# Optimization experiments

Measured on AMD Instinct MI355X. Metric: run time of the kernel, lower is better.

Reference implementation:

```python
import jax, jax.numpy as jnp
import numpy as np

B, S, H, N = 2, 2048, 1024, 16
D = H // N


def setup_inputs() -> dict:
    key = jax.random.key(0)
    k1, k2, k3 = jax.random.split(key, 3)
    # Xavier-uniform-ish init for projection weights
    lim_in = (6.0 / (H + 3 * H)) ** 0.5
    lim_out = (6.0 / (H + H)) ** 0.5
    return {
        "hidden_states": jax.random.normal(k1, (B, S, H), dtype=jnp.float32),
        "w_in": jax.random.uniform(k2, (3 * H, H), minval=-lim_in, maxval=lim_in, dtype=jnp.float32),
        "b_in": jnp.zeros((3 * H,), dtype=jnp.float32),
        "w_out": jax.random.uniform(k3, (H, H), minval=-lim_out, maxval=lim_out, dtype=jnp.float32),
        "b_out": jnp.zeros((H,), dtype=jnp.float32),
    }


def reference(hidden_states, w_in, b_in, w_out, b_out):
    b, s, h = hidden_states.shape
    qkv = hidden_states @ w_in.T + b_in  # [B,S,3H]
    q, k, v = jnp.split(qkv, 3, axis=-1)
    # [B,S,H] -> [B,N,S,D]
    def to_heads(x):
        return x.reshape(b, s, N, D).transpose(0, 2, 1, 3)
    q, k, v = to_heads(q), to_heads(k), to_heads(v)
    scale = D ** -0.5
    scores = jnp.einsum("bnqd,bnkd->bnqk", q, k) * scale  # [B,N,S,S]
    causal = jnp.triu(jnp.ones((s, s), dtype=bool), k=1)
    scores = jnp.where(causal, -jnp.inf, scores)
    attn = jax.nn.softmax(scores, axis=-1)
    out = jnp.einsum("bnqk,bnkd->bnqd", attn, v)  # [B,N,S,D]
    out = out.transpose(0, 2, 1, 3).reshape(b, s, h)
    return out @ w_out.T + b_out
```

## Files before the change

### kernel.cpp

```cpp
#include <hip/hip_runtime.h>
#include <hip/hip_bf16.h>

#define BB 2
#define SS 2048
#define HH 1024
#define NH 16
#define DD 64
#define H3 3072
#define MM (BB*SS)

typedef unsigned short u16;
typedef unsigned int u32;
typedef __attribute__((ext_vector_type(8))) short bf16x8;
typedef __attribute__((ext_vector_type(4))) float f32x4;
typedef __attribute__((ext_vector_type(16))) float f32x16;

__device__ __forceinline__ u16 f2bf(float f) {
    union { float f; u32 u; } v; v.f = f;
    u32 u = v.u;
    u += 0x7fffu + ((u >> 16) & 1u);
    return (u16)(u >> 16);
}
__device__ __forceinline__ float bf2f(u16 h) {
    union { u32 u; float f; } v; v.u = ((u32)h) << 16;
    return v.f;
}
__device__ __forceinline__ u32 pack2bf(float a, float b) {
    __hip_bfloat162 h = __float22bfloat162_rn(float2{a, b});
    u32 u; __builtin_memcpy(&u, &h, 4);
    return u;
}
__device__ __forceinline__ void gl_lds16(const void* g, void* l) {
    __builtin_amdgcn_global_load_lds(
        (const __attribute__((address_space(1))) u32*)g,
        (__attribute__((address_space(3))) u32*)l, 16, 0, 0);
}

__global__ void cvt3bf(const float4* __restrict__ s0, uint2* __restrict__ d0, int n0,
                       const float4* __restrict__ s1, uint2* __restrict__ d1, int n1,
                       const float4* __restrict__ s2, uint2* __restrict__ d2, int n2) {
    int i = blockIdx.x * blockDim.x + threadIdx.x;
    const int tot = n0 + n1 + n2;
    for (; i < tot; i += gridDim.x * blockDim.x) {
        const float4* s; uint2* d; int j;
        if (i < n0)            { s = s0; d = d0; j = i; }
        else if (i < n0 + n1)  { s = s1; d = d1; j = i - n0; }
        else                   { s = s2; d = d2; j = i - n0 - n1; }
        float4 v = s[j];
        uint2 o; o.x = pack2bf(v.x, v.y); o.y = pack2bf(v.z, v.w);
        d[j] = o;
    }
}

template<int BN, int MODE>
__global__ __launch_bounds__(256, 2)
void gemm_k2(const u16* __restrict__ A, const u16* __restrict__ Bbf,
             const u16* __restrict__ biasbf, void* __restrict__ Cptr,
             u16* __restrict__ Qo, u16* __restrict__ Ko, u16* __restrict__ Vto,
             int M, int Nn, int K)
{
    constexpr int NFR = BN / 32;
    __shared__ __align__(16) u16 Alds[128 * 32];
    __shared__ __align__(16) u16 Blds[BN * 32];
    const int tid = threadIdx.x;
    const int w = tid >> 6, lane = tid & 63, quad = lane >> 4, l16 = lane & 15;
    const int m0 = blockIdx.x * 128, n0 = blockIdx.y * BN;
    const int wm = w >> 1, wn = w & 1;
    const int rA4 = lane >> 2, c8b = (lane & 3) * 8;

    f32x4 acc[4][NFR] = {};

    for (int k0 = 0; k0 < K; k0 += 32) {
        __syncthreads();
#pragma unroll
        for (int q = 0; q < 2; ++q) {
            int row0 = w * 32 + q * 16;
            gl_lds16(&A[(size_t)(m0 + row0 + rA4) * K + k0 + c8b], &Alds[row0 * 32]);
        }
#pragma unroll
        for (int q = 0; q < BN / 64; ++q) {
            int row0 = w * (BN / 4) + q * 16;
            gl_lds16(&Bbf[(size_t)(n0 + row0 + rA4) * K + k0 + c8b], &Blds[row0 * 32]);
        }
        __syncthreads();

        bf16x8 af[4], bfr[NFR];
#pragma unroll
        for (int mi = 0; mi < 4; ++mi)
            af[mi] = *(const bf16x8*)&Alds[(wm * 64 + mi * 16 + l16) * 32 + quad * 8];
#pragma unroll
        for (int ni = 0; ni < NFR; ++ni)
            bfr[ni] = *(const bf16x8*)&Blds[(wn * (BN / 2) + ni * 16 + l16) * 32 + quad * 8];
#pragma unroll
        for (int mi = 0; mi < 4; ++mi)
#pragma unroll
            for (int ni = 0; ni < NFR; ++ni)
                acc[mi][ni] = __builtin_amdgcn_mfma_f32_16x16x32_bf16(
                    af[mi], bfr[ni], acc[mi][ni], 0, 0, 0);
    }

#pragma unroll
    for (int mi = 0; mi < 4; ++mi) {
        int row_b = m0 + wm * 64 + mi * 16 + quad * 4;
#pragma unroll
        for (int ni = 0; ni < NFR; ++ni) {
            int col = n0 + wn * (BN / 2) + ni * 16 + l16;
            float bv = bf2f(biasbf[col]);
            if constexpr (MODE == 1) {
#pragma unroll
                for (int i = 0; i < 4; ++i)
                    ((float*)Cptr)[(size_t)(row_b + i) * Nn + col] = acc[mi][ni][i] + bv;
            } else {
                if (col < 1024) {
#pragma unroll
                    for (int i = 0; i < 4; ++i)
                        Qo[(size_t)(row_b + i) * 1024 + col] =
                            f2bf((acc[mi][ni][i] + bv) * 0.125f);
                } else if (col < 2048) {
#pragma unroll
                    for (int i = 0; i < 4; ++i)
                        Ko[(size_t)(row_b + i) * 1024 + (col - 1024)] =
                            f2bf(acc[mi][ni][i] + bv);
                } else {
                    int d = col - 2048, hh = d >> 6, dd = d & 63;
                    int b = row_b >> 11, s = row_b & 2047;
                    u16 t0 = f2bf(acc[mi][ni][0] + bv), t1 = f2bf(acc[mi][ni][1] + bv);
                    u16 t2 = f2bf(acc[mi][ni][2] + bv), t3 = f2bf(acc[mi][ni][3] + bv);
                    uint2 pk; pk.x = (u32)t0 | ((u32)t1 << 16);
                    pk.y = (u32)t2 | ((u32)t3 << 16);
                    *(uint2*)&Vto[((size_t)((b * 16 + hh) * 64 + dd)) * 2048 + s] = pk;
                }
            }
        }
    }
}

__global__ __launch_bounds__(256, 2)
void attn_v4(const u16* __restrict__ Q, const u16* __restrict__ Kb,
             const u16* __restrict__ Vt, u16* __restrict__ attn_out) {
    const int qt = 15 - blockIdx.x, h = blockIdx.y, b = blockIdx.z;
    const int tid = threadIdx.x;
    const int w = tid >> 6, lane = tid & 63;
    const int l32 = lane & 31, h5 = lane >> 5;
    __shared__ __align__(16) u16 Klds[2][64 * 72];
    __shared__ __align__(16) u16 Vlds[2][64 * 72];
    __shared__ __align__(16) u16 Pb[4][32 * 72];
    const int r0 = tid >> 3, cc8 = (tid & 7) * 8;

    const int q0 = qt * 128;
    const int qw = q0 + w * 32;
    const int T = 2 * (qt + 1);

    const u16* Qb = Q  + (size_t)(b * SS) * 1024 + h * 64;
    const u16* Kg = Kb + (size_t)(b * SS) * 1024 + h * 64;
    const u16* Vg = Vt + (size_t)((b * 16 + h) * 64) * 2048;

    bf16x8 qf[4];
#pragma unroll
    for (int kt = 0; kt < 4; ++kt)
        qf[kt] = *(const bf16x8*)&Qb[(size_t)(qw + l32) * 1024 + kt * 16 + h5 * 8];

    f32x16 oacc[2] = {};
    float lp[16];
#pragma unroll
    for (int j = 0; j < 16; ++j) lp[j] = 0.f;

    uint4 kr0 = *(const uint4*)&Kg[(size_t)r0 * 1024 + cc8];
    uint4 kr1 = *(const uint4*)&Kg[(size_t)(r0 + 32) * 1024 + cc8];
    uint4 vr0 = *(const uint4*)&Vg[(size_t)r0 * 2048 + cc8];
    uint4 vr1 = *(const uint4*)&Vg[(size_t)(r0 + 32) * 2048 + cc8];
    *(uint4*)&Klds[0][r0 * 72 + cc8]        = kr0;
    *(uint4*)&Klds[0][(r0 + 32) * 72 + cc8] = kr1;
    *(uint4*)&Vlds[0][r0 * 72 + cc8]        = vr0;
    *(uint4*)&Vlds[0][(r0 + 32) * 72 + cc8] = vr1;

    for (int t = 0; t < T; ++t) {
        const int cur = t & 1;
        const int kv0 = t * 64;
        __syncthreads();
        if (t + 1 < T) {
            const int nv = kv0 + 64;
            kr0 = *(const uint4*)&Kg[(size_t)(nv + r0) * 1024 + cc8];
            kr1 = *(const uint4*)&Kg[(size_t)(nv + r0 + 32) * 1024 + cc8];
            vr0 = *(const uint4*)&Vg[(size_t)r0 * 2048 + nv + cc8];
            vr1 = *(const uint4*)&Vg[(size_t)(r0 + 32) * 2048 + nv + cc8];
        }
        f32x16 sacc[2] = {};
#pragma unroll
        for (int nt = 0; nt < 2; ++nt)
#pragma unroll
            for (int kt = 0; kt < 4; ++kt) {
                bf16x8 kf = *(const bf16x8*)
                    &Klds[cur][(nt * 32 + l32) * 72 + kt * 16 + h5 * 8];
                sacc[nt] = __builtin_amdgcn_mfma_f32_32x32x16_bf16(
                    qf[kt], kf, sacc[nt], 0, 0, 0);
            }
#pragma unroll
        for (int nt = 0; nt < 2; ++nt) {
            int colg = kv0 + nt * 32 + l32;
#pragma unroll
            for (int j = 0; j < 16; ++j) {
                int rl = (j & 3) + 8 * (j >> 2) + 4 * h5;
                float p = (colg <= qw + rl) ? __expf(sacc[nt][j]) : 0.f;
                lp[j] += p;
                Pb[w][rl * 72 + nt * 32 + l32] = f2bf(p);
            }
        }
#pragma unroll
        for (int kt = 0; kt < 4; ++kt) {
            bf16x8 pa = *(const bf16x8*)&Pb[w][l32 * 72 + kt * 16 + h5 * 8];
#pragma unroll
            for (int nt = 0; nt < 2; ++nt) {
                bf16x8 vf = *(const bf16x8*)
                    &Vlds[cur][(nt * 32 + l32) * 72 + kt * 16 + h5 * 8];
                oacc[nt] = __builtin_amdgcn_mfma_f32_32x32x16_bf16(
                    pa, vf, oacc[nt], 0, 0, 0);
            }
        }
        if (t + 1 < T) {
            const int nxt = cur ^ 1;
            *(uint4*)&Klds[nxt][r0 * 72 + cc8]        = kr0;
            *(uint4*)&Klds[nxt][(r0 + 32) * 72 + cc8] = kr1;
            *(uint4*)&Vlds[nxt][r0 * 72 + cc8]        = vr0;
            *(uint4*)&Vlds[nxt][(r0 + 32) * 72 + cc8] = vr1;
        }
    }

#pragma unroll
    for (int j = 0; j < 16; ++j) {
#pragma unroll
        for (int s = 1; s < 32; s <<= 1)
            lp[j] += __shfl_xor(lp[j], s, 64);
        lp[j] = 1.0f / lp[j];
    }
    u16* ob = attn_out + (size_t)(b * SS + qw) * 1024 + h * 64;
#pragma unroll
    for (int nt = 0; nt < 2; ++nt)
#pragma unroll
        for (int j = 0; j < 16; ++j) {
            int rl = (j & 3) + 8 * (j >> 2) + 4 * h5;
            ob[(size_t)rl * 1024 + nt * 32 + l32] = f2bf(oacc[nt][j] * lp[j]);
        }
}

extern "C" void kernel_launch(void* const* d_in, const int* in_sizes, int n_in,
                              void* d_out, int out_size, void* d_ws, size_t ws_size,
                              hipStream_t stream) {
    const float* hidden = (const float*)d_in[0];
    const float* w_in   = (const float*)d_in[1];
    const float* b_in   = (const float*)d_in[2];
    const float* w_out  = (const float*)d_in[3];
    const float* b_out  = (const float*)d_in[4];
    float* out = (float*)d_out;

    char* ws = (char*)d_ws;
    u16* hid_bf  = (u16*)d_out;
    u16* wi_bf   = (u16*)ws;
    u16* bi_bf   = (u16*)(ws + 6291456);
    u16* attn_ws = (u16*)ws;
    u16* Qbuf    = (u16*)(ws + 8388608);
    u16* wo_bf   = (u16*)(ws + 8388608);
    u16* bo_bf   = (u16*)(ws + 8388608 + 2097152);
    u16* Kbuf    = (u16*)(ws + 16777216);
    u16* Vtbuf   = (u16*)(ws + 25165824);

    cvt3bf<<<dim3(2048), dim3(256), 0, stream>>>(
        (const float4*)hidden, (uint2*)hid_bf, 1048576,
        (const float4*)w_in,   (uint2*)wi_bf,  786432,
        (const float4*)b_in,   (uint2*)bi_bf,  768);
    gemm_k2<128, 2><<<dim3(32, 24), dim3(256), 0, stream>>>(
        hid_bf, wi_bf, bi_bf, nullptr, Qbuf, Kbuf, Vtbuf, MM, H3, HH);
    attn_v4<<<dim3(16, NH, BB), dim3(256), 0, stream>>>(
        Qbuf, Kbuf, Vtbuf, attn_ws);
    cvt3bf<<<dim3(512), dim3(256), 0, stream>>>(
        (const float4*)w_out, (uint2*)wo_bf, 262144,
        (const float4*)b_out, (uint2*)bo_bf, 256,
        nullptr, nullptr, 0);
    gemm_k2<64, 1><<<dim3(32, 16), dim3(256), 0, stream>>>(
        attn_ws, wo_bf, bo_bf, out, nullptr, nullptr, nullptr, MM, HH, HH);
}
```

Before: 202.0 us.

## Rework attention: paired causal query tiles, split-KV across warps, direct global loads

Each attention block now handles two 64-row query tiles, one long and one short, paired so that causal work per block is balanced. The four warps split into two query groups times two KV parities, and partial outputs and row sums are combined through shared memory. K and V fragments are read straight from global memory instead of through a double-buffered LDS stage, and the causal mask is applied only on the diagonal tile. This balances work across blocks and removes per-iteration barriers, at the cost of uncoalesced, unshared global K/V loads that now rely on cache hits.

```diff
diff --git a/kernel.cpp b/kernel.cpp
--- a/kernel.cpp
+++ b/kernel.cpp
@@ -136,111 +136,124 @@
 }
 
 __global__ __launch_bounds__(256, 2)
-void attn_v4(const u16* __restrict__ Q, const u16* __restrict__ Kb,
+void attn_v6(const u16* __restrict__ Q, const u16* __restrict__ Kb,
              const u16* __restrict__ Vt, u16* __restrict__ attn_out) {
-    const int qt = 15 - blockIdx.x, h = blockIdx.y, b = blockIdx.z;
+    const int pr = blockIdx.x, h = blockIdx.y, b = blockIdx.z;
     const int tid = threadIdx.x;
     const int w = tid >> 6, lane = tid & 63;
     const int l32 = lane & 31, h5 = lane >> 5;
-    __shared__ __align__(16) u16 Klds[2][64 * 72];
-    __shared__ __align__(16) u16 Vlds[2][64 * 72];
+    const int wq = w & 1;
+    const int wp = w >> 1;
+
     __shared__ __align__(16) u16 Pb[4][32 * 72];
-    const int r0 = tid >> 3, cc8 = (tid & 7) * 8;
-
-    const int q0 = qt * 128;
-    const int qw = q0 + w * 32;
-    const int T = 2 * (qt + 1);
-
-    const u16* Qb = Q  + (size_t)(b * SS) * 1024 + h * 64;
+    __shared__ float Oc[2][32 * 68];
+    __shared__ float lc[2][32];
+
+    const u16* Qg = Q  + (size_t)(b * SS) * 1024 + h * 64;
     const u16* Kg = Kb + (size_t)(b * SS) * 1024 + h * 64;
     const u16* Vg = Vt + (size_t)((b * 16 + h) * 64) * 2048;
 
-    bf16x8 qf[4];
-#pragma unroll
-    for (int kt = 0; kt < 4; ++kt)
-        qf[kt] = *(const bf16x8*)&Qb[(size_t)(qw + l32) * 1024 + kt * 16 + h5 * 8];
-
-    f32x16 oacc[2] = {};
-    float lp[16];
-#pragma unroll
-    for (int j = 0; j < 16; ++j) lp[j] = 0.f;
-
-    uint4 kr0 = *(const uint4*)&Kg[(size_t)r0 * 1024 + cc8];
-    uint4 kr1 = *(const uint4*)&Kg[(size_t)(r0 + 32) * 1024 + cc8];
-    uint4 vr0 = *(const uint4*)&Vg[(size_t)r0 * 2048 + cc8];
-    uint4 vr1 = *(const uint4*)&Vg[(size_t)(r0 + 32) * 2048 + cc8];
-    *(uint4*)&Klds[0][r0 * 72 + cc8]        = kr0;
-    *(uint4*)&Klds[0][(r0 + 32) * 72 + cc8] = kr1;
-    *(uint4*)&Vlds[0][r0 * 72 + cc8]        = vr0;
-    *(uint4*)&Vlds[0][(r0 + 32) * 72 + cc8] = vr1;
-
-    for (int t = 0; t < T; ++t) {
-        const int cur = t & 1;
-        const int kv0 = t * 64;
-        __syncthreads();
-        if (t + 1 < T) {
-            const int nv = kv0 + 64;
-            kr0 = *(const uint4*)&Kg[(size_t)(nv + r0) * 1024 + cc8];
-            kr1 = *(const uint4*)&Kg[(size_t)(nv + r0 + 32) * 1024 + cc8];
-            vr0 = *(const uint4*)&Vg[(size_t)r0 * 2048 + nv + cc8];
-            vr1 = *(const uint4*)&Vg[(size_t)(r0 + 32) * 2048 + nv + cc8];
-        }
-        f32x16 sacc[2] = {};
-#pragma unroll
-        for (int nt = 0; nt < 2; ++nt)
+    for (int half = 0; half < 2; ++half) {
+        const int qt = half ? pr : (31 - pr);
+        const int q0 = qt * 64;
+        const int qw = q0 + wq * 32;
+        const int T = qt + 1;
+
+        bf16x8 qf[4];
+#pragma unroll
+        for (int kt = 0; kt < 4; ++kt)
+            qf[kt] = *(const bf16x8*)&Qg[(size_t)(qw + l32) * 1024 + kt * 16 + h5 * 8];
+
+        f32x16 oacc[2] = {};
+        float lp[16];
+#pragma unroll
+        for (int j = 0; j < 16; ++j) lp[j] = 0.f;
+
+        for (int t = wp; t < T; t += 2) {
+            const int kv0 = t * 64;
+            f32x16 sacc[2] = {};
+#pragma unroll
+            for (int nt = 0; nt < 2; ++nt)
+#pragma unroll
+                for (int kt = 0; kt < 4; ++kt) {
+                    bf16x8 kf = *(const bf16x8*)
+                        &Kg[(size_t)(kv0 + nt * 32 + l32) * 1024 + kt * 16 + h5 * 8];
+                    sacc[nt] = __builtin_amdgcn_mfma_f32_32x32x16_bf16(
+                        qf[kt], kf, sacc[nt], 0, 0, 0);
+                }
+            if (t == qt) {
+#pragma unroll
+                for (int nt = 0; nt < 2; ++nt) {
+                    int colg = kv0 + nt * 32 + l32;
+#pragma unroll
+                    for (int j = 0; j < 16; ++j) {
+                        int rl = (j & 3) + 8 * (j >> 2) + 4 * h5;
+                        float p = (colg <= qw + rl) ? __expf(sacc[nt][j]) : 0.f;
+                        lp[j] += p;
+                        Pb[w][rl * 72 + nt * 32 + l32] = f2bf(p);
+                    }
+                }
+            } else {
+#pragma unroll
+                for (int nt = 0; nt < 2; ++nt)
+#pragma unroll
+                    for (int j = 0; j < 16; ++j) {
+                        int rl = (j & 3) + 8 * (j >> 2) + 4 * h5;
+                        float p = __expf(sacc[nt][j]);
+                        lp[j] += p;
+                        Pb[w][rl * 72 + nt * 32 + l32] = f2bf(p);
+                    }
+            }
 #pragma unroll
             for (int kt = 0; kt < 4; ++kt) {
-                bf16x8 kf = *(const bf16x8*)
-                    &Klds[cur][(nt * 32 + l32) * 72 + kt * 16 + h5 * 8];
-                sacc[nt] = __builtin_amdgcn_mfma_f32_32x32x16_bf16(
-                    qf[kt], kf, sacc[nt], 0, 0, 0);
-            }
-#pragma unroll
-        for (int nt = 0; nt < 2; ++nt) {
-            int colg = kv0 + nt * 32 + l32;
+                bf16x8 pa = *(const bf16x8*)&Pb[w][l32 * 72 + kt * 16 + h5 * 8];
+#pragma unroll
+                for (int nt = 0; nt < 2; ++nt) {
+                    bf16x8 vf = *(const bf16x8*)
+                        &Vg[(size_t)(nt * 32 + l32) * 2048 + kv0 + kt * 16 + h5 * 8];
+                    oacc[nt] = __builtin_amdgcn_mfma_f32_32x32x16_bf16(
+                        pa, vf, oacc[nt], 0, 0, 0);
+                }
+            }
+        }
+
+#pragma unroll
+        for (int j = 0; j < 16; ++j)
+#pragma unroll
+            for (int s = 1; s < 32; s <<= 1)
+                lp[j] += __shfl_xor(lp[j], s, 64);
+
+        if (wp == 1) {
+#pragma unroll
+            for (int nt = 0; nt < 2; ++nt)
+#pragma unroll
+                for (int j = 0; j < 16; ++j) {
+                    int rl = (j & 3) + 8 * (j >> 2) + 4 * h5;
+                    Oc[wq][rl * 68 + nt * 32 + l32] = oacc[nt][j];
+                }
+            if (l32 == 0)
+#pragma unroll
+                for (int j = 0; j < 16; ++j) {
+                    int rl = (j & 3) + 8 * (j >> 2) + 4 * h5;
+                    lc[wq][rl] = lp[j];
+                }
+        }
+        __syncthreads();
+        if (wp == 0) {
+            u16* ob = attn_out + (size_t)(b * SS + qw) * 1024 + h * 64;
 #pragma unroll
             for (int j = 0; j < 16; ++j) {
                 int rl = (j & 3) + 8 * (j >> 2) + 4 * h5;
-                float p = (colg <= qw + rl) ? __expf(sacc[nt][j]) : 0.f;
-                lp[j] += p;
-                Pb[w][rl * 72 + nt * 32 + l32] = f2bf(p);
-            }
-        }
-#pragma unroll
-        for (int kt = 0; kt < 4; ++kt) {
-            bf16x8 pa = *(const bf16x8*)&Pb[w][l32 * 72 + kt * 16 + h5 * 8];
-#pragma unroll
-            for (int nt = 0; nt < 2; ++nt) {
-                bf16x8 vf = *(const bf16x8*)
-                    &Vlds[cur][(nt * 32 + l32) * 72 + kt * 16 + h5 * 8];
-                oacc[nt] = __builtin_amdgcn_mfma_f32_32x32x16_bf16(
-                    pa, vf, oacc[nt], 0, 0, 0);
-            }
-        }
-        if (t + 1 < T) {
-            const int nxt = cur ^ 1;
-            *(uint4*)&Klds[nxt][r0 * 72 + cc8]        = kr0;
-            *(uint4*)&Klds[nxt][(r0 + 32) * 72 + cc8] = kr1;
-            *(uint4*)&Vlds[nxt][r0 * 72 + cc8]        = vr0;
-            *(uint4*)&Vlds[nxt][(r0 + 32) * 72 + cc8] = vr1;
-        }
-    }
-
-#pragma unroll
-    for (int j = 0; j < 16; ++j) {
-#pragma unroll
-        for (int s = 1; s < 32; s <<= 1)
-            lp[j] += __shfl_xor(lp[j], s, 64);
-        lp[j] = 1.0f / lp[j];
-    }
-    u16* ob = attn_out + (size_t)(b * SS + qw) * 1024 + h * 64;
-#pragma unroll
-    for (int nt = 0; nt < 2; ++nt)
-#pragma unroll
-        for (int j = 0; j < 16; ++j) {
-            int rl = (j & 3) + 8 * (j >> 2) + 4 * h5;
-            ob[(size_t)rl * 1024 + nt * 32 + l32] = f2bf(oacc[nt][j] * lp[j]);
-        }
+                float linv = 1.0f / (lp[j] + lc[wq][rl]);
+#pragma unroll
+                for (int nt = 0; nt < 2; ++nt) {
+                    float v = (oacc[nt][j] + Oc[wq][rl * 68 + nt * 32 + l32]) * linv;
+                    ob[(size_t)rl * 1024 + nt * 32 + l32] = f2bf(v);
+                }
+            }
+        }
+        __syncthreads();
+    }
 }
 
 extern "C" void kernel_launch(void* const* d_in, const int* in_sizes, int n_in,
@@ -270,7 +283,7 @@
         (const float4*)b_in,   (uint2*)bi_bf,  768);
     gemm_k2<128, 2><<<dim3(32, 24), dim3(256), 0, stream>>>(
         hid_bf, wi_bf, bi_bf, nullptr, Qbuf, Kbuf, Vtbuf, MM, H3, HH);
-    attn_v4<<<dim3(16, NH, BB), dim3(256), 0, stream>>>(
+    attn_v6<<<dim3(16, NH, BB), dim3(256), 0, stream>>>(
         Qbuf, Kbuf, Vtbuf, attn_ws);
     cvt3bf<<<dim3(512), dim3(256), 0, stream>>>(
         (const float4*)w_out, (uint2*)wo_bf, 262144,
```

New measurement: 215.3 us. 1.07x slower.
